# Performance work log

Hardware: AMD Instinct MI355X
Metric: run time of the kernel (lower is better)

Reference implementation:

```python
import jax, jax.numpy as jnp
import numpy as np

B, IN_DIM, N, L = 8, 2, 512, 64
D_MODEL = 32
D_FF = 32          # must equal D_MODEL: output_bn is BatchNorm2d(d_model) applied to skip
DEPTH = 3          # blocks=3 * layers=1; dilation resets to 1 each block -> all dilations = 1
KS = 2             # temporal kernel size
EPS = 1e-5         # BatchNorm eps


def setup_inputs() -> dict:
    key = jax.random.key(0)
    ks = jax.random.split(key, 16)
    s = 0.1  # weight scale for numeric sanity
    x = jax.random.normal(ks[0], (B, IN_DIM, N, L), jnp.float32)
    a = jax.random.uniform(ks[1], (N, N), jnp.float32)
    adj = a / a.sum(axis=1, keepdims=True)  # row-stochastic diffusion matrix
    return {
        "x": x,
        "adj": adj,
        "Wstart": jax.random.normal(ks[2], (D_MODEL, IN_DIM), jnp.float32) * s,
        "bstart": jnp.zeros((D_MODEL,), jnp.float32),
        "Wf": jax.random.normal(ks[3], (DEPTH, D_MODEL, D_MODEL, KS), jnp.float32) * s,
        "bf": jnp.zeros((DEPTH, D_MODEL), jnp.float32),
        "Wg": jax.random.normal(ks[4], (DEPTH, D_MODEL, D_MODEL, KS), jnp.float32) * s,
        "bg": jnp.zeros((DEPTH, D_MODEL), jnp.float32),
        "Wskip": jax.random.normal(ks[5], (DEPTH, D_FF, D_MODEL), jnp.float32) * s,
        "bskip": jnp.zeros((DEPTH, D_FF), jnp.float32),
        "Wgc": jax.random.normal(ks[6], (DEPTH, D_MODEL, 3 * D_MODEL), jnp.float32) * s,
        "bgc": jnp.zeros((DEPTH, D_MODEL), jnp.float32),
        "gcbn_g": jnp.ones((DEPTH, D_MODEL), jnp.float32),
        "gcbn_b": jnp.zeros((DEPTH, D_MODEL), jnp.float32),
        "bn_g": jnp.ones((DEPTH, D_MODEL), jnp.float32),
        "bn_b": jnp.zeros((DEPTH, D_MODEL), jnp.float32),
        "obn_g": jnp.ones((D_MODEL,), jnp.float32),
        "obn_b": jnp.zeros((D_MODEL,), jnp.float32),
    }


def _c1x1(x, W, b):
    # Conv2d with (1,1) kernel == channel mixing. x: [b,c,n,l], W: [o,c]
    return jnp.einsum('bcnl,oc->bonl', x, W) + b[None, :, None, None]


def _dconv(x, W, b, d):
    # Conv2d kernel (1,2), dilation d along time (valid). W: [o,c,2]
    Lx = x.shape[-1]
    y = (jnp.einsum('bcnl,oc->bonl', x[..., :Lx - d], W[..., 0])
         + jnp.einsum('bcnl,oc->bonl', x[..., d:], W[..., 1]))
    return y + b[None, :, None, None]


def _bn(x, g, bta):
    # eval-mode BatchNorm2d: running_mean=0, running_var=1
    inv = g / jnp.sqrt(1.0 + EPS)
    return x * inv[None, :, None, None] + bta[None, :, None, None]


def reference(x, adj, Wstart, bstart, Wf, bf, Wg, bg, Wskip, bskip,
              Wgc, bgc, gcbn_g, gcbn_b, bn_g, bn_b, obn_g, obn_b):
    rf = 1 + DEPTH * (KS - 1)  # receptive field with dilation 1 per layer
    h = _c1x1(x, Wstart, bstart)
    if h.shape[-1] < rf:
        h = jnp.pad(h, ((0, 0), (0, 0), (0, 0), (rf - h.shape[-1], 0)))
    skip = None
    for i in range(DEPTH):
        residual = h
        filt = jnp.tanh(_dconv(h, Wf[i], bf[i], 1))
        gate = jax.nn.sigmoid(_dconv(h, Wg[i], bg[i], 1))
        h = filt * gate
        s = _c1x1(h, Wskip[i], bskip[i])
        skip = s if skip is None else s + skip[..., -s.shape[-1]:]
        if i == DEPTH - 1:
            break
        # order-2 graph diffusion: h, A h, A^2 h -> concat -> 1x1 conv -> BN (dropout: eval noop)
        x1 = jnp.einsum('bcnl,nm->bcml', h, adj)
        x2 = jnp.einsum('bcnl,nm->bcml', x1, adj)
        cat = jnp.concatenate([h, x1, x2], axis=1)
        g = _bn(_c1x1(cat, Wgc[i], bgc[i]), gcbn_g[i], gcbn_b[i])
        h = g + residual[..., -g.shape[-1]:]
        h = _bn(h, bn_g[i], bn_b[i])
    out = _bn(skip, obn_g, obn_b)
    return jnp.swapaxes(out, 1, 3)  # [B, L', N, C]
```

## Files before the change

kernel.cpp:

```cpp
#include <hip/hip_runtime.h>
#include <hip/hip_bf16.h>

#define B_     8
#define CIN_   2
#define N_     512
#define C_     32
#define L_     64
#define LOUT_  61
#define BUF_   ((size_t)(8*32*512*64))

typedef __hip_bfloat16 bf16;
typedef unsigned short ushort_t;
typedef __attribute__((ext_vector_type(8))) unsigned short us8;
typedef __attribute__((ext_vector_type(8))) short bf16x8;
typedef __attribute__((ext_vector_type(4))) float f32x4;

static __device__ __forceinline__ float bits2f(ushort_t u) {
    return __uint_as_float(((unsigned)u) << 16);
}
static __device__ __forceinline__ ushort_t f2bits(float v) {
    unsigned u = __float_as_uint(v);
    return (ushort_t)((u + 0x7fffu + ((u >> 16) & 1u)) >> 16);
}

__global__ void k_start(const float* __restrict__ x,
                        const float* __restrict__ Wst,
                        const float* __restrict__ bst,
                        ushort_t* __restrict__ h) {
    int idx = blockIdx.x * 256 + threadIdx.x;
    int l0 = (idx & 7) * 8;
    int n  = (idx >> 3) & 511;
    int o  = (idx >> 12) & 31;
    int b  = idx >> 17;
    float w0 = Wst[o * 2], w1 = Wst[o * 2 + 1], bb = bst[o];
    int xbase = (b * CIN_ * N_ + n) * L_ + l0;
    float va[8], vb[8];
    *(float4*)&va[0] = *(const float4*)(x + xbase);
    *(float4*)&va[4] = *(const float4*)(x + xbase + 4);
    *(float4*)&vb[0] = *(const float4*)(x + xbase + N_ * L_);
    *(float4*)&vb[4] = *(const float4*)(x + xbase + N_ * L_ + 4);
    us8 r;
    #pragma unroll
    for (int k = 0; k < 8; ++k) r[k] = f2bits(bb + va[k] * w0 + vb[k] * w1);
    *(us8*)(h + (size_t)idx * 8) = r;
}

__global__ void k_transA(const float* __restrict__ adj, ushort_t* __restrict__ adjT) {
    __shared__ float buf[64][65];
    int ti = blockIdx.x & 7;
    int tj = blockIdx.x >> 3;
    int t = threadIdx.x;
    for (int r = 0; r < 16; ++r) {
        int e = t + 256 * r;
        int rl = e >> 6, cl = e & 63;
        buf[rl][cl] = adj[(size_t)(ti * 64 + rl) * 512 + tj * 64 + cl];
    }
    __syncthreads();
    for (int r = 0; r < 16; ++r) {
        int e = t + 256 * r;
        int ml = e >> 6, nl = e & 63;
        adjT[(size_t)(tj * 64 + ml) * 512 + ti * 64 + nl] = f2bits(buf[nl][ml]);
    }
}

__global__ __launch_bounds__(256, 2) void k_sq(const ushort_t* __restrict__ adjT,
                                               ushort_t* __restrict__ adj2T) {
    __shared__ __align__(16) ushort_t lds2[8192];
    ushort_t* As = lds2;
    ushort_t* Bs = lds2 + 4096;
    int mt = blockIdx.x & 7, nc = blockIdx.x >> 3;
    int t = threadIdx.x, lane = t & 63, w = t >> 6;
    int la = lane & 15, q = lane >> 4;
    f32x4 acc[4];
    #pragma unroll
    for (int mi = 0; mi < 4; ++mi) acc[mi] = (f32x4)0.f;
    for (int p0 = 0; p0 < 512; p0 += 64) {
        __syncthreads();
        #pragma unroll
        for (int r = 0; r < 2; ++r) {
            int e = t + 256 * r, ml = e >> 3, oct = e & 7;
            int sw = ((oct + (ml >> 3)) & 7) << 3;
            *(us8*)(As + ml * 64 + sw) =
                *(const us8*)(adjT + (size_t)(mt * 64 + ml) * 512 + p0 + oct * 8);
            *(us8*)(Bs + ml * 64 + sw) =
                *(const us8*)(adjT + (size_t)(p0 + ml) * 512 + nc * 64 + oct * 8);
        }
        __syncthreads();
        #pragma unroll
        for (int ks = 0; ks < 2; ++ks) {
            bf16x8 a[4];
            #pragma unroll
            for (int mi = 0; mi < 4; ++mi) {
                int m = mi * 16 + la;
                int bl = (ks * 4 + q + (m >> 3)) & 7;
                a[mi] = *(const bf16x8*)(As + m * 64 + bl * 8);
            }
            bf16x8 bv;
            {
                int n = w * 16 + la;
                int rot = ((n >> 3) + ks * 4 + q) & 7;
                int col = rot * 8 + (n & 7);
                const ushort_t* p = Bs + (ks * 32 + q * 8) * 64 + col;
                #pragma unroll
                for (int j = 0; j < 8; ++j) bv[j] = (short)p[j * 64];
            }
            #pragma unroll
            for (int mi = 0; mi < 4; ++mi)
                acc[mi] = __builtin_amdgcn_mfma_f32_16x16x32_bf16(a[mi], bv, acc[mi], 0, 0, 0);
        }
    }
    __syncthreads();
    ushort_t* Ys = lds2;
    #pragma unroll
    for (int mi = 0; mi < 4; ++mi)
        #pragma unroll
        for (int r = 0; r < 4; ++r)
            Ys[(mi * 16 + q * 4 + r) * 72 + w * 16 + la] = f2bits(acc[mi][r]);
    __syncthreads();
    #pragma unroll
    for (int r = 0; r < 2; ++r) {
        int e = t + 256 * r, ml = e >> 3, oct = e & 7;
        us8 v = *(const us8*)(Ys + ml * 72 + oct * 8);
        *(us8*)(adj2T + (size_t)(mt * 64 + ml) * 512 + nc * 64 + oct * 8) = v;
    }
}

__global__ __launch_bounds__(256, 2) void k_gs_mfma(
        const ushort_t* __restrict__ h,
        const float* __restrict__ Wf, const float* __restrict__ bfp,
        const float* __restrict__ Wg, const float* __restrict__ bgp,
        const float* __restrict__ Wsk, const float* __restrict__ bsk,
        ushort_t* __restrict__ G, float* __restrict__ out,
        int off, int mode, int storeG,
        const float* __restrict__ og, const float* __restrict__ obb) {
    __shared__ __align__(16) ushort_t Hs[128 * 72];
    __shared__ __align__(16) ushort_t Asf[32 * 72];
    __shared__ __align__(16) ushort_t Asg[32 * 72];
    __shared__ __align__(16) ushort_t As2[32 * 40];
    __shared__ float bfv[32], bgv[32], bsv[32];
    int t = threadIdx.x;
    int b = blockIdx.x >> 7, n0 = (blockIdx.x & 127) * 4;
    int lane = t & 63, w = t >> 6;
    int la = lane & 15, q = lane >> 4;

    {
        int o = t >> 3, k8 = (t & 7) * 8;
        us8 vf, vg;
        #pragma unroll
        for (int i = 0; i < 8; ++i) {
            int k = k8 + i, c = k & 31, tap = k >> 5;
            vf[i] = f2bits(Wf[o * 64 + c * 2 + tap]);
            vg[i] = f2bits(Wg[o * 64 + c * 2 + tap]);
        }
        *(us8*)(Asf + o * 72 + k8) = vf;
        *(us8*)(Asg + o * 72 + k8) = vg;
        if (k8 < 32) {
            us8 vs;
            #pragma unroll
            for (int i = 0; i < 8; ++i) vs[i] = f2bits(Wsk[o * 32 + k8 + i]);
            *(us8*)(As2 + o * 40 + k8) = vs;
        }
        if (t < 32) { bfv[t] = bfp[t]; bgv[t] = bgp[t]; bsv[t] = bsk[t]; }
    }
    const ushort_t* hb = h + (size_t)(b * 32) * 512 * 64;
    #pragma unroll
    for (int r = 0; r < 4; ++r) {
        int e = t + 256 * r;
        int row = e >> 3, oct = e & 7;
        us8 v = *(const us8*)(hb + ((size_t)(row >> 2) * 512 + n0 + (row & 3)) * 64 + oct * 8);
        int sw = (oct + row + (row >> 5)) & 7;
        *(us8*)(Hs + row * 72 + sw * 8) = v;
    }
    {
        int row = t >> 1, hf = t & 1;
        *(uint2*)(Hs + row * 72 + 64 + hf * 4) = make_uint2(0u, 0u);
    }
    __syncthreads();

    bf16x8 af[2][2], ag[2][2];
    #pragma unroll
    for (int mt = 0; mt < 2; ++mt)
        #pragma unroll
        for (int ks = 0; ks < 2; ++ks) {
            af[mt][ks] = *(const bf16x8*)(Asf + (mt * 16 + la) * 72 + ks * 32 + q * 8);
            ag[mt][ks] = *(const bf16x8*)(Asg + (mt * 16 + la) * 72 + ks * 32 + q * 8);
        }

    f32x4 fa[2][4], ga[2][4];
    #pragma unroll
    for (int mt = 0; mt < 2; ++mt)
        #pragma unroll
        for (int ct = 0; ct < 4; ++ct) { fa[mt][ct] = (f32x4)0.f; ga[mt][ct] = (f32x4)0.f; }
    #pragma unroll
    for (int ct = 0; ct < 4; ++ct) {
        #pragma unroll
        for (int ks = 0; ks < 2; ++ks) {
            int le = ct * 16 + la + ks;
            bf16x8 bv;
            #pragma unroll
            for (int j = 0; j < 8; ++j) {
                int row = 32 * q + 4 * j + w;
                int pos = (le < 64) ? ((((le >> 3) + row + q) & 7) * 8 + (le & 7)) : le;
                bv[j] = (short)Hs[row * 72 + pos];
            }
            #pragma unroll
            for (int mt = 0; mt < 2; ++mt) {
                fa[mt][ct] = __builtin_amdgcn_mfma_f32_16x16x32_bf16(af[mt][ks], bv, fa[mt][ct], 0, 0, 0);
                ga[mt][ct] = __builtin_amdgcn_mfma_f32_16x16x32_bf16(ag[mt][ks], bv, ga[mt][ct], 0, 0, 0);
            }
        }
    }

    #pragma unroll
    for (int mt = 0; mt < 2; ++mt)
        #pragma unroll
        for (int ct = 0; ct < 4; ++ct)
            #pragma unroll
            for (int r = 0; r < 4; ++r) {
                int o = mt * 16 + q * 4 + r;
                float fv = fa[mt][ct][r] + bfv[o];
                float gv = ga[mt][ct][r] + bgv[o];
                float ef = __expf(2.f * fv);
                float act = (1.f - 2.f / (ef + 1.f)) * (1.f / (1.f + __expf(-gv)));
                int l = ct * 16 + la;
                int row = o * 4 + w;
                int sw = ((l >> 3) + row + (row >> 5)) & 7;
                Hs[row * 72 + sw * 8 + (l & 7)] = f2bits(act);
            }

    bf16x8 a2[2];
    a2[0] = *(const bf16x8*)(As2 + la * 40 + q * 8);
    a2[1] = *(const bf16x8*)(As2 + (16 + la) * 40 + q * 8);
    f32x4 sa[2][4];
    #pragma unroll
    for (int mt = 0; mt < 2; ++mt)
        #pragma unroll
        for (int ct = 0; ct < 4; ++ct) sa[mt][ct] = (f32x4)0.f;
    #pragma unroll
    for (int ct = 0; ct < 4; ++ct) {
        int le = ct * 16 + la + off;
        bf16x8 bv;
        #pragma unroll
        for (int j = 0; j < 8; ++j) {
            int row = 32 * q + 4 * j + w;
            int pos = (le < 64) ? ((((le >> 3) + row + q) & 7) * 8 + (le & 7)) : le;
            bv[j] = (short)Hs[row * 72 + pos];
        }
        sa[0][ct] = __builtin_amdgcn_mfma_f32_16x16x32_bf16(a2[0], bv, sa[0][ct], 0, 0, 0);
        sa[1][ct] = __builtin_amdgcn_mfma_f32_16x16x32_bf16(a2[1], bv, sa[1][ct], 0, 0, 0);
    }
    __syncthreads();

    if (storeG) {
        #pragma unroll
        for (int r = 0; r < 4; ++r) {
            int e = t + 256 * r;
            int row = e >> 3, oct = e & 7;
            int sw = (oct + row + (row >> 5)) & 7;
            us8 v = *(const us8*)(Hs + row * 72 + sw * 8);
            *(us8*)(G + ((size_t)(b * 32 + (row >> 2)) * 512 + n0 + (row & 3)) * 64 + oct * 8) = v;
        }
    }
    __syncthreads();

    float* St = (float*)Hs;
    const float rbn = rsqrtf(1.f + 1e-5f);
    #pragma unroll
    for (int half = 0; half < 2; ++half) {
        if ((w >> 1) == half) {
            #pragma unroll
            for (int mt = 0; mt < 2; ++mt)
                #pragma unroll
                for (int ct = 0; ct < 4; ++ct) {
                    int col = (w & 1) * 64 + ct * 16 + la;
                    int ob = mt * 16 + q * 4;
                    float4 sv = make_float4(sa[mt][ct][0] + bsv[ob],
                                            sa[mt][ct][1] + bsv[ob + 1],
                                            sa[mt][ct][2] + bsv[ob + 2],
                                            sa[mt][ct][3] + bsv[ob + 3]);
                    *(float4*)(St + col * 36 + ob) = sv;
                }
        }
        __syncthreads();
        {
            int col = t >> 1, o0 = (t & 1) * 16;
            int nr = half * 2 + (col >> 6), l = col & 63;
            if (l < LOUT_) {
                float* po = out + ((size_t)(b * LOUT_ + l) * 512 + n0 + nr) * 32 + o0;
                #pragma unroll
                for (int i = 0; i < 4; ++i) {
                    float4 s = *(float4*)(St + col * 36 + o0 + i * 4);
                    if (mode == 0) {
                        *(float4*)(po + i * 4) = s;
                    } else {
                        float4 old = *(float4*)(po + i * 4);
                        float4 vv = make_float4(old.x + s.x, old.y + s.y,
                                                old.z + s.z, old.w + s.w);
                        if (mode == 2) {
                            int ob = o0 + i * 4;
                            vv.x = vv.x * (og[ob] * rbn) + obb[ob];
                            vv.y = vv.y * (og[ob + 1] * rbn) + obb[ob + 1];
                            vv.z = vv.z * (og[ob + 2] * rbn) + obb[ob + 2];
                            vv.w = vv.w * (og[ob + 3] * rbn) + obb[ob + 3];
                        }
                        *(float4*)(po + i * 4) = vv;
                    }
                }
            }
        }
        __syncthreads();
    }
}

__global__ __launch_bounds__(256, 2) void k_diffuse2(
        const ushort_t* __restrict__ X, const ushort_t* __restrict__ adjT,
        const ushort_t* __restrict__ adj2T,
        ushort_t* __restrict__ Y1, ushort_t* __restrict__ Y2) {
    __shared__ __align__(16) ushort_t lds[16384];
    ushort_t* As1 = lds;
    ushort_t* As2 = lds + 4096;
    ushort_t* Xs  = lds + 8192;
    int cp = blockIdx.x & 15;
    int mt = (blockIdx.x >> 4) & 7;
    int b  = blockIdx.x >> 7;
    int t  = threadIdx.x;
    int lane = t & 63, w = t >> 6;
    int c_loc = w & 1, lh = w >> 1;
    int m0 = mt * 64;
    int la = lane & 15, q = lane >> 4;
    const ushort_t* Xb = X + (size_t)(b * 32 + cp * 2) * 512 * 64;
    f32x4 acc1[4][2], acc2[4][2];
    #pragma unroll
    for (int mi = 0; mi < 4; ++mi)
        #pragma unroll
        for (int li = 0; li < 2; ++li) { acc1[mi][li] = (f32x4)0.f; acc2[mi][li] = (f32x4)0.f; }

    for (int n0 = 0; n0 < 512; n0 += 64) {
        __syncthreads();
        #pragma unroll
        for (int r = 0; r < 2; ++r) {
            int e = t + 256 * r;
            int ml = e >> 3, oct = e & 7;
            int sw = ((oct + (ml >> 3)) & 7) << 3;
            *(us8*)(As1 + ml * 64 + sw) =
                *(const us8*)(adjT + (size_t)(m0 + ml) * 512 + n0 + oct * 8);
            *(us8*)(As2 + ml * 64 + sw) =
                *(const us8*)(adj2T + (size_t)(m0 + ml) * 512 + n0 + oct * 8);
        }
        #pragma unroll
        for (int r = 0; r < 4; ++r) {
            int e = t + 256 * r;
            int cl = e >> 9, nl = (e >> 3) & 63, oct = e & 7;
            us8 v = *(const us8*)(Xb + ((size_t)cl * 512 + n0 + nl) * 64 + oct * 8);
            *(us8*)(Xs + cl * 4096 + nl * 64 + (((oct + (nl >> 3)) & 7) << 3)) = v;
        }
        __syncthreads();
        #pragma unroll
        for (int ks = 0; ks < 2; ++ks) {
            bf16x8 a1[4], a2v[4];
            #pragma unroll
            for (int mi = 0; mi < 4; ++mi) {
                int m = mi * 16 + la;
                int bl = (ks * 4 + q + (m >> 3)) & 7;
                a1[mi]  = *(const bf16x8*)(As1 + m * 64 + bl * 8);
                a2v[mi] = *(const bf16x8*)(As2 + m * 64 + bl * 8);
            }
            bf16x8 bb[2];
            #pragma unroll
            for (int li = 0; li < 2; ++li) {
                int l = lh * 32 + li * 16 + la;
                int rot = ((l >> 3) + ks * 4 + q) & 7;
                int col = rot * 8 + (l & 7);
                const ushort_t* p = Xs + c_loc * 4096 + (ks * 32 + q * 8) * 64 + col;
                bf16x8 v;
                #pragma unroll
                for (int j = 0; j < 8; ++j) v[j] = (short)p[j * 64];
                bb[li] = v;
            }
            #pragma unroll
            for (int mi = 0; mi < 4; ++mi)
                #pragma unroll
                for (int li = 0; li < 2; ++li) {
                    acc1[mi][li] = __builtin_amdgcn_mfma_f32_16x16x32_bf16(a1[mi], bb[li], acc1[mi][li], 0, 0, 0);
                    acc2[mi][li] = __builtin_amdgcn_mfma_f32_16x16x32_bf16(a2v[mi], bb[li], acc2[mi][li], 0, 0, 0);
                }
        }
    }
    ushort_t* Ys = lds;
    #pragma unroll
    for (int pass = 0; pass < 2; ++pass) {
        __syncthreads();
        f32x4 (*src)[2] = pass ? acc2 : acc1;
        #pragma unroll
        for (int mi = 0; mi < 4; ++mi)
            #pragma unroll
            for (int li = 0; li < 2; ++li)
                #pragma unroll
                for (int r = 0; r < 4; ++r) {
                    int row = mi * 16 + q * 4 + r;
                    int col = lh * 32 + li * 16 + la;
                    Ys[c_loc * 4608 + row * 72 + col] = f2bits(src[mi][li][r]);
                }
        __syncthreads();
        ushort_t* Yo = pass ? Y2 : Y1;
        int c = t >> 7, mrem = t & 127;
        int m = mrem >> 1, lq = mrem & 1;
        #pragma unroll
        for (int r = 0; r < 4; ++r) {
            int l0 = lq * 32 + r * 8;
            us8 v = *(const us8*)(Ys + c * 4608 + m * 72 + l0);
            *(us8*)(Yo + ((size_t)(b * 32 + cp * 2 + c) * 512 + m0 + m) * 64 + l0) = v;
        }
    }
}

__global__ __launch_bounds__(256, 2) void k_gc3_mfma(
        ushort_t* __restrict__ G, const ushort_t* __restrict__ X1,
        const ushort_t* __restrict__ X2, const ushort_t* __restrict__ hres,
        const float* __restrict__ Wgc, const float* __restrict__ bgc,
        const float* __restrict__ gg, const float* __restrict__ gb,
        const float* __restrict__ bg2, const float* __restrict__ bb2) {
    __shared__ __align__(16) ushort_t cat[384 * 72];
    __shared__ __align__(16) ushort_t hr[128 * 64];
    __shared__ __align__(16) ushort_t Aw[32 * 104];
    __shared__ float prm[5][32];
    int t = threadIdx.x;
    int b = blockIdx.x >> 7, n0 = (blockIdx.x & 127) * 4;
    int lane = t & 63, w = t >> 6;
    int la = lane & 15, q = lane >> 4;

    #pragma unroll
    for (int r = 0; r < 12; ++r) {
        int e = t + 256 * r;
        int row = e >> 3, oct = e & 7;
        int k = row >> 2;
        const ushort_t* src = (k < 32) ? G : ((k < 64) ? X1 : X2);
        us8 v = *(const us8*)(src + ((size_t)(b * 32 + (k & 31)) * 512 + n0 + (row & 3)) * 64 + oct * 8);
        int sw = (oct + row + (row >> 5)) & 7;
        *(us8*)(cat + row * 72 + sw * 8) = v;
    }
    #pragma unroll
    for (int r = 0; r < 4; ++r) {
        int e = t + 256 * r;
        int row = e >> 3, oct = e & 7;
        us8 v = *(const us8*)(hres + ((size_t)(b * 32 + (row >> 2)) * 512 + n0 + (row & 3)) * 64 + oct * 8);
        *(us8*)(hr + row * 64 + oct * 8) = v;
    }
    for (int e = t; e < 384; e += 256) {
        int o = e / 12, oct = e % 12;
        us8 v;
        #pragma unroll
        for (int i = 0; i < 8; ++i) v[i] = f2bits(Wgc[o * 96 + oct * 8 + i]);
        *(us8*)(Aw + o * 104 + oct * 8) = v;
    }
    if (t < 32) {
        prm[0][t] = bgc[t]; prm[1][t] = gg[t]; prm[2][t] = gb[t];
        prm[3][t] = bg2[t]; prm[4][t] = bb2[t];
    }
    __syncthreads();

    bf16x8 a[2][3];
    #pragma unroll
    for (int mt = 0; mt < 2; ++mt)
        #pragma unroll
        for (int ks = 0; ks < 3; ++ks)
            a[mt][ks] = *(const bf16x8*)(Aw + (mt * 16 + la) * 104 + ks * 32 + q * 8);

    f32x4 acc[2][4];
    #pragma unroll
    for (int mt = 0; mt < 2; ++mt)
        #pragma unroll
        for (int ct = 0; ct < 4; ++ct) acc[mt][ct] = (f32x4)0.f;
    #pragma unroll
    for (int ct = 0; ct < 4; ++ct) {
        int le = ct * 16 + la;
        #pragma unroll
        for (int ks = 0; ks < 3; ++ks) {
            bf16x8 bv;
            #pragma unroll
            for (int j = 0; j < 8; ++j) {
                int row = (ks * 32 + q * 8 + j) * 4 + w;
                int sw = ((le >> 3) + row + (row >> 5)) & 7;
                bv[j] = (short)cat[row * 72 + sw * 8 + (le & 7)];
            }
            acc[0][ct] = __builtin_amdgcn_mfma_f32_16x16x32_bf16(a[0][ks], bv, acc[0][ct], 0, 0, 0);
            acc[1][ct] = __builtin_amdgcn_mfma_f32_16x16x32_bf16(a[1][ks], bv, acc[1][ct], 0, 0, 0);
        }
    }
    __syncthreads();

    const float rbn = rsqrtf(1.f + 1e-5f);
    #pragma unroll
    for (int mt = 0; mt < 2; ++mt)
        #pragma unroll
        for (int ct = 0; ct < 4; ++ct)
            #pragma unroll
            for (int r = 0; r < 4; ++r) {
                int o = mt * 16 + q * 4 + r;
                int l = ct * 16 + la;
                float v = acc[mt][ct][r] + prm[0][o];
                v = v * (prm[1][o] * rbn) + prm[2][o];
                float res = (l < 63) ? bits2f(hr[(o * 4 + w) * 64 + l + 1]) : 0.f;
                v = (v + res) * (prm[3][o] * rbn) + prm[4][o];
                int row = o * 4 + w;
                int sw = ((l >> 3) + row + (row >> 5)) & 7;
                cat[row * 72 + sw * 8 + (l & 7)] = f2bits(v);
            }
    __syncthreads();
    #pragma unroll
    for (int r = 0; r < 4; ++r) {
        int e = t + 256 * r;
        int row = e >> 3, oct = e & 7;
        int sw = (oct + row + (row >> 5)) & 7;
        us8 v = *(const us8*)(cat + row * 72 + sw * 8);
        *(us8*)(G + ((size_t)(b * 32 + (row >> 2)) * 512 + n0 + (row & 3)) * 64 + oct * 8) = v;
    }
}

extern "C" void kernel_launch(void* const* d_in, const int* in_sizes, int n_in,
                              void* d_out, int out_size, void* d_ws, size_t ws_size,
                              hipStream_t stream) {
    const float* x      = (const float*)d_in[0];
    const float* adj    = (const float*)d_in[1];
    const float* Wstart = (const float*)d_in[2];
    const float* bstart = (const float*)d_in[3];
    const float* Wf     = (const float*)d_in[4];
    const float* bf_    = (const float*)d_in[5];
    const float* Wg     = (const float*)d_in[6];
    const float* bg     = (const float*)d_in[7];
    const float* Wskip  = (const float*)d_in[8];
    const float* bskip  = (const float*)d_in[9];
    const float* Wgc    = (const float*)d_in[10];
    const float* bgc    = (const float*)d_in[11];
    const float* gcbn_g = (const float*)d_in[12];
    const float* gcbn_b = (const float*)d_in[13];
    const float* bn_g   = (const float*)d_in[14];
    const float* bn_b   = (const float*)d_in[15];
    const float* obn_g  = (const float*)d_in[16];
    const float* obn_b  = (const float*)d_in[17];
    float* out = (float*)d_out;

    ushort_t* P0    = (ushort_t*)d_ws;
    ushort_t* P1    = P0 + BUF_;
    ushort_t* P2    = P1 + BUF_;
    ushort_t* P3    = P2 + BUF_;
    ushort_t* adjT  = P3 + BUF_;
    ushort_t* adj2T = adjT + 512 * 512;

    k_transA<<<64, 256, 0, stream>>>(adj, adjT);
    k_sq<<<64, 256, 0, stream>>>(adjT, adj2T);
    k_start<<<4096, 256, 0, stream>>>(x, Wstart, bstart, P0);

    ushort_t* h  = P0;
    ushort_t* Gb = P1;
    for (int i = 0; i < 3; ++i) {
        int mode = (i == 0) ? 0 : ((i == 2) ? 2 : 1);
        k_gs_mfma<<<1024, 256, 0, stream>>>(h, Wf + i * 2048, bf_ + i * 32,
                                            Wg + i * 2048, bg + i * 32,
                                            Wskip + i * 1024, bskip + i * 32,
                                            Gb, out, 2 - i, mode, (i < 2) ? 1 : 0,
                                            obn_g, obn_b);
        if (i == 2) break;
        k_diffuse2<<<1024, 256, 0, stream>>>(Gb, adjT, adj2T, P2, P3);
        k_gc3_mfma<<<1024, 256, 0, stream>>>(Gb, P2, P3, h,
                                             Wgc + i * 3072, bgc + i * 32,
                                             gcbn_g + i * 32, gcbn_b + i * 32,
                                             bn_g + i * 32, bn_b + i * 32);
        ushort_t* tmp = h; h = Gb; Gb = tmp;
    }
}
```

Baseline: 318.4 us.

## Load diffusion tiles via global_load_lds and build B fragments with DPP swaps

The diffusion GEMM kernel now copies adjacency and activation tiles straight from global memory into LDS with global_load_lds, with the swizzle moved onto the source address instead of the LDS destination. This avoids staging the data through registers. The B-fragment gather, previously eight scalar 16-bit LDS reads per fragment, is replaced by four 32-bit reads per lane, a DPP lane swap and byte permutes. This cuts LDS instruction count but adds VALU work and relies on the lane-pairing layout being correct.

```diff
diff --git a/kernel.cpp b/kernel.cpp
--- a/kernel.cpp
+++ b/kernel.cpp
@@ -11,6 +11,7 @@
 
 typedef __hip_bfloat16 bf16;
 typedef unsigned short ushort_t;
+typedef unsigned int u32;
 typedef __attribute__((ext_vector_type(8))) unsigned short us8;
 typedef __attribute__((ext_vector_type(8))) short bf16x8;
 typedef __attribute__((ext_vector_type(4))) float f32x4;
@@ -21,6 +22,17 @@
 static __device__ __forceinline__ ushort_t f2bits(float v) {
     unsigned u = __float_as_uint(v);
     return (ushort_t)((u + 0x7fffu + ((u >> 16) & 1u)) >> 16);
+}
+
+static __device__ __forceinline__ void gload16(const ushort_t* g, ushort_t* l) {
+    __builtin_amdgcn_global_load_lds(
+        (const __attribute__((address_space(1))) unsigned int*)g,
+        (__attribute__((address_space(3))) unsigned int*)l,
+        16, 0, 0);
+}
+
+static __device__ __forceinline__ u32 swap1(u32 v) {
+    return (u32)__builtin_amdgcn_update_dpp(0, (int)v, 0xB1, 0xF, 0xF, true);
 }
 
 __global__ void k_start(const float* __restrict__ x,
@@ -328,6 +340,8 @@
     int c_loc = w & 1, lh = w >> 1;
     int m0 = mt * 64;
     int la = lane & 15, q = lane >> 4;
+    int p_ = la & 1;
+    u32 sel = p_ ? 0x07060302u : 0x05040100u;
     const ushort_t* Xb = X + (size_t)(b * 32 + cp * 2) * 512 * 64;
     f32x4 acc1[4][2], acc2[4][2];
     #pragma unroll
@@ -335,26 +349,26 @@
         #pragma unroll
         for (int li = 0; li < 2; ++li) { acc1[mi][li] = (f32x4)0.f; acc2[mi][li] = (f32x4)0.f; }
 
+    union U { u32 u[4]; bf16x8 v; };
+
     for (int n0 = 0; n0 < 512; n0 += 64) {
         __syncthreads();
         #pragma unroll
         for (int r = 0; r < 2; ++r) {
-            int e = t + 256 * r;
-            int ml = e >> 3, oct = e & 7;
-            int sw = ((oct + (ml >> 3)) & 7) << 3;
-            *(us8*)(As1 + ml * 64 + sw) =
-                *(const us8*)(adjT + (size_t)(m0 + ml) * 512 + n0 + oct * 8);
-            *(us8*)(As2 + ml * 64 + sw) =
-                *(const us8*)(adj2T + (size_t)(m0 + ml) * 512 + n0 + oct * 8);
+            int e = t + 256 * r, ml = e >> 3, s = e & 7;
+            int og = ((s - (ml >> 3)) & 7) * 8;
+            gload16(adjT  + (size_t)(m0 + ml) * 512 + n0 + og, As1 + (size_t)e * 8);
+            gload16(adj2T + (size_t)(m0 + ml) * 512 + n0 + og, As2 + (size_t)e * 8);
         }
         #pragma unroll
         for (int r = 0; r < 4; ++r) {
             int e = t + 256 * r;
-            int cl = e >> 9, nl = (e >> 3) & 63, oct = e & 7;
-            us8 v = *(const us8*)(Xb + ((size_t)cl * 512 + n0 + nl) * 64 + oct * 8);
-            *(us8*)(Xs + cl * 4096 + nl * 64 + (((oct + (nl >> 3)) & 7) << 3)) = v;
-        }
-        __syncthreads();
+            int cl = e >> 9, nl = (e >> 3) & 63, s = e & 7;
+            int og = ((s - (nl >> 3)) & 7) * 8;
+            gload16(Xb + ((size_t)cl * 512 + n0 + nl) * 64 + og, Xs + (size_t)e * 8);
+        }
+        __syncthreads();
+
         #pragma unroll
         for (int ks = 0; ks < 2; ++ks) {
             bf16x8 a1[4], a2v[4];
@@ -368,20 +382,28 @@
             bf16x8 bb[2];
             #pragma unroll
             for (int li = 0; li < 2; ++li) {
-                int l = lh * 32 + li * 16 + la;
-                int rot = ((l >> 3) + ks * 4 + q) & 7;
-                int col = rot * 8 + (l & 7);
-                const ushort_t* p = Xs + c_loc * 4096 + (ks * 32 + q * 8) * 64 + col;
-                bf16x8 v;
-                #pragma unroll
-                for (int j = 0; j < 8; ++j) v[j] = (short)p[j * 64];
-                bb[li] = v;
+                int l2 = lh * 32 + li * 16 + (la & ~1);
+                int r0 = ks * 32 + q * 8 + p_ * 4;
+                int rot = ((l2 >> 3) + ks * 4 + q) & 7;
+                const u32* bp = (const u32*)(Xs + c_loc * 4096 + r0 * 64 + rot * 8 + (l2 & 7));
+                u32 o0 = bp[0], o1 = bp[32], o2 = bp[64], o3 = bp[96];
+                u32 s0 = swap1(o0), s1 = swap1(o1), s2 = swap1(o2), s3 = swap1(o3);
+                u32 lo0 = p_ ? s0 : o0, lo1 = p_ ? s1 : o1;
+                u32 lo2 = p_ ? s2 : o2, lo3 = p_ ? s3 : o3;
+                u32 hi0 = p_ ? o0 : s0, hi1 = p_ ? o1 : s1;
+                u32 hi2 = p_ ? o2 : s2, hi3 = p_ ? o3 : s3;
+                U u;
+                u.u[0] = __builtin_amdgcn_perm(lo1, lo0, sel);
+                u.u[1] = __builtin_amdgcn_perm(lo3, lo2, sel);
+                u.u[2] = __builtin_amdgcn_perm(hi1, hi0, sel);
+                u.u[3] = __builtin_amdgcn_perm(hi3, hi2, sel);
+                bb[li] = u.v;
             }
             #pragma unroll
             for (int mi = 0; mi < 4; ++mi)
                 #pragma unroll
                 for (int li = 0; li < 2; ++li) {
-                    acc1[mi][li] = __builtin_amdgcn_mfma_f32_16x16x32_bf16(a1[mi], bb[li], acc1[mi][li], 0, 0, 0);
+                    acc1[mi][li] = __builtin_amdgcn_mfma_f32_16x16x32_bf16(a1[mi],  bb[li], acc1[mi][li], 0, 0, 0);
                     acc2[mi][li] = __builtin_amdgcn_mfma_f32_16x16x32_bf16(a2v[mi], bb[li], acc2[mi][li], 0, 0, 0);
                 }
         }
```

Measured after the change: 317.4 us. Within noise of the previous version (-0.3%).
